# Performance work log

Hardware: AMD Instinct MI355X
Metric: run time of the kernel (lower is better)

The kernel has to match this reference:

```python
import jax, jax.numpy as jnp
import numpy as np

WIN = 7  # window size (w1 = w2 = 7)

def _rel_pos_indices(w: int) -> jnp.ndarray:
    # Matches RelPosBias 2-D branch: [(w*w), (w*w)] indices into (2w-1)^2 table
    p = np.arange(w)
    gi, gj = np.meshgrid(p, p, indexing='ij')
    grid = np.stack([gi.reshape(-1), gj.reshape(-1)], axis=-1)  # [w*w, 2]
    rel = grid[:, None, :] - grid[None, :, :]                   # [w*w, w*w, 2]
    rel = rel + (w - 1)
    idx = rel[..., 0] * (2 * w - 1) + rel[..., 1]               # [w*w, w*w]
    return jnp.asarray(idx, dtype=jnp.int32)


def setup_inputs() -> dict:
    key = jax.random.key(0)
    k1, k2, k3, k4 = jax.random.split(key, 4)
    dim, heads = 256, 8
    b, gx, gy = 64, 8, 8
    x = jax.random.normal(k1, (b, gx, gy, WIN, WIN, dim), dtype=jnp.float32)
    # torch nn.Linear weight layout: [out_features, in_features]
    w_qkv = jax.random.normal(k2, (3 * dim, dim), dtype=jnp.float32) * (dim ** -0.5)
    w_out = jax.random.normal(k3, (dim, dim), dtype=jnp.float32) * (dim ** -0.5)
    rel_emb = jax.random.normal(k4, ((2 * WIN - 1) ** 2, heads), dtype=jnp.float32) * 0.02
    rel_idx = _rel_pos_indices(WIN)
    return {"x": x, "w_qkv": w_qkv, "w_out": w_out, "rel_emb": rel_emb, "rel_idx": rel_idx}


def reference(x, w_qkv, w_out, rel_emb, rel_idx):
    b, gx, gy, w1, w2, d = x.shape
    h = rel_emb.shape[1]          # heads
    dh = d // h                    # dim_head
    scale = dh ** -0.5
    n = w1 * w2                    # tokens per window (49)

    xr = x.reshape(b * gx * gy, n, d)                        # (B, n, d)
    qkv = jnp.einsum('bnd,ed->bne', xr, w_qkv)               # (B, n, 3d)
    q, k, v = jnp.split(qkv, 3, axis=-1)
    split_heads = lambda t: t.reshape(t.shape[0], n, h, dh).transpose(0, 2, 1, 3)
    q, k, v = map(split_heads, (q, k, v))                    # (B, h, n, dh)

    sim = jnp.einsum('bhid,bhjd->bhij', q * scale, k)        # (B, h, n, n)
    bias = rel_emb[rel_idx]                                   # (n, n, h)
    sim = sim + bias.transpose(2, 0, 1)[None]                 # + (1, h, n, n)
    attn = jax.nn.softmax(sim, axis=-1)

    out = jnp.einsum('bhij,bhjd->bhid', attn, v)              # (B, h, n, dh)
    out = out.transpose(0, 2, 1, 3).reshape(-1, w1, w2, d)    # (B, w1, w2, d)
    out = jnp.einsum('bxyd,ed->bxye', out, w_out)
    return out.reshape(b, gx, gy, w1, w2, d)
```

## Files before the change

### kernel.cpp

```cpp
#include <hip/hip_runtime.h>
#include <hip/hip_bf16.h>

typedef __bf16 bf16x8 __attribute__((ext_vector_type(8)));
typedef __bf16 bf16x4v __attribute__((ext_vector_type(4)));
typedef float f32x4 __attribute__((ext_vector_type(4)));

#define MFMA(a, b, c) __builtin_amdgcn_mfma_f32_16x16x32_bf16((a), (b), (c), 0, 0, 0)
#define NEG_BIG (-1e30f)

#define XO_LD 264
#define QK_LD 36
#define VT_LD 72
#define P_LD 68
#define OTR_LD 36
#define Q_OFF 0
#define K_OFF 2304
#define VT_OFF 4608
#define P_OFF 6912
#define OTR_OFF 11264
#define TOTAL_ELS (64 * XO_LD)

static __device__ inline bf16x8 ld8x2(const __bf16* p) {
  bf16x4v lo = *(const bf16x4v*)p;
  bf16x4v hi = *(const bf16x4v*)(p + 4);
  bf16x8 r;
  r[0] = lo[0]; r[1] = lo[1]; r[2] = lo[2]; r[3] = lo[3];
  r[4] = hi[0]; r[5] = hi[1]; r[6] = hi[2]; r[7] = hi[3];
  return r;
}

__global__ __launch_bounds__(256) void prep_kernel(
    const float* __restrict__ w_qkv, const float* __restrict__ w_out,
    const float* __restrict__ rel_emb, const int* __restrict__ rel_idx,
    __bf16* __restrict__ wqkv_f, __bf16* __restrict__ wout_f,
    float* __restrict__ bias) {
  const float kScale = 0.17677669529663687f;
  int idx = blockIdx.x * 256 + threadIdx.x;
  if (idx < 24576) {
    int lane = idx & 63, k2 = (idx >> 6) & 7;
    int hn = idx >> 9;
    int nt = hn % 6, h = hn / 6;
    int quad = lane >> 4, l16 = lane & 15;
    int grow = (nt >> 1) * 256 + h * 32 + (nt & 1) * 16 + l16;
    const float* src = w_qkv + grow * 256 + k2 * 32 + quad * 8;
    float s = (nt < 2) ? kScale : 1.0f;
    bf16x8 d;
#pragma unroll
    for (int j = 0; j < 8; ++j) d[j] = (__bf16)(src[j] * s);
    *(bf16x8*)&wqkv_f[idx * 8] = d;
  } else if (idx < 32768) {
    int j2 = idx - 24576;
    int lane = j2 & 63, kk = (j2 >> 6) & 7, ntile = j2 >> 9;
    int quad = lane >> 4, l16 = lane & 15;
    const float* src = w_out + (ntile * 16 + l16) * 256 + kk * 32 + quad * 8;
    bf16x8 d;
#pragma unroll
    for (int j = 0; j < 8; ++j) d[j] = (__bf16)src[j];
    *(bf16x8*)&wout_f[j2 * 8] = d;
  } else if (idx < 65536) {
    int j = idx - 32768;
    int h = j >> 12;
    int mt = (j >> 10) & 3;
    int nt = (j >> 8) & 3;
    int lane = (j >> 2) & 63;
    int r = j & 3;
    int row = mt * 16 + ((lane >> 4) << 2) + r;
    int col = nt * 16 + (lane & 15);
    float v = NEG_BIG;
    if (row < 49 && col < 49) v = rel_emb[rel_idx[row * 49 + col] * 8 + h];
    bias[j] = v;
  }
}

__global__ __launch_bounds__(256, 4) void attn_kernel(
    const float* __restrict__ x, const __bf16* __restrict__ wqkv,
    const __bf16* __restrict__ wout, const float* __restrict__ bias,
    float* __restrict__ out) {
  __shared__ __attribute__((aligned(16))) __bf16 sm[TOTAL_ELS];

  const int tid = threadIdx.x;
  const int wave = tid >> 6;
  const int lane = tid & 63;
  const int quad = lane >> 4;
  const int l16 = lane & 15;
  const int i0 = wave * 16 + quad * 4;
  const int am = wave * 16 + l16;

  const f32x4 fzero = {0.f, 0.f, 0.f, 0.f};

  {
    const float4* xg = (const float4*)(x + (size_t)blockIdx.x * 12544);
    for (int i = tid; i < 3136; i += 256) {
      float4 v = xg[i];
      int row = i >> 6, c4 = (i & 63) << 2;
      bf16x4v t;
      t[0] = (__bf16)v.x; t[1] = (__bf16)v.y; t[2] = (__bf16)v.z; t[3] = (__bf16)v.w;
      *(bf16x4v*)&sm[row * XO_LD + c4] = t;
    }
    bf16x4v z;
    z[0] = z[1] = z[2] = z[3] = (__bf16)0.0f;
    for (int i = tid; i < 960; i += 256) {
      int row = 49 + (i >> 6), c4 = (i & 63) << 2;
      *(bf16x4v*)&sm[row * XO_LD + c4] = z;
    }
  }
  __syncthreads();

  bf16x8 afr[8];
#pragma unroll
  for (int kk = 0; kk < 8; ++kk)
    afr[kk] = *(const bf16x8*)&sm[am * XO_LD + kk * 32 + quad * 8];
  __syncthreads();

  bf16x8 ofr[8];

  for (int h = 0; h < 8; ++h) {
    f32x4 acc[6];
#pragma unroll
    for (int t = 0; t < 6; ++t) acc[t] = fzero;
    {
      const __bf16* wb = wqkv + (size_t)h * 24576;
#pragma unroll
      for (int k2 = 0; k2 < 8; ++k2) {
        bf16x8 a = afr[k2];
#pragma unroll
        for (int nt = 0; nt < 6; ++nt) {
          bf16x8 b = *(const bf16x8*)&wb[(nt * 8 + k2) * 512 + lane * 8];
          acc[nt] = MFMA(a, b, acc[nt]);
        }
      }
    }

    f32x4 sim[4];
    {
      const float* bb = bias + (h << 12) + (wave << 10) + (lane << 2);
#pragma unroll
      for (int nt = 0; nt < 4; ++nt) sim[nt] = *(const f32x4*)&bb[nt << 8];
    }

#pragma unroll
    for (int t = 0; t < 2; ++t) {
#pragma unroll
      for (int r = 0; r < 4; ++r) {
        sm[Q_OFF + (i0 + r) * QK_LD + t * 16 + l16] = (__bf16)acc[t][r];
        sm[K_OFF + (i0 + r) * QK_LD + t * 16 + l16] = (__bf16)acc[2 + t][r];
      }
      bf16x4v pv;
#pragma unroll
      for (int r = 0; r < 4; ++r) pv[r] = (__bf16)acc[4 + t][r];
      *(bf16x4v*)&sm[VT_OFF + (t * 16 + l16) * VT_LD + i0] = pv;
    }
    __syncthreads();

    {
      bf16x8 a = ld8x2(&sm[Q_OFF + am * QK_LD + quad * 8]);
#pragma unroll
      for (int nt = 0; nt < 4; ++nt) {
        bf16x8 b = ld8x2(&sm[K_OFF + (nt * 16 + l16) * QK_LD + quad * 8]);
        sim[nt] = MFMA(a, b, sim[nt]);
      }
    }

#pragma unroll
    for (int r = 0; r < 4; ++r) {
      float mx = fmaxf(fmaxf(sim[0][r], sim[1][r]), fmaxf(sim[2][r], sim[3][r]));
      mx = fmaxf(mx, __shfl_xor(mx, 1));
      mx = fmaxf(mx, __shfl_xor(mx, 2));
      mx = fmaxf(mx, __shfl_xor(mx, 4));
      mx = fmaxf(mx, __shfl_xor(mx, 8));
      float e0 = __expf(sim[0][r] - mx), e1 = __expf(sim[1][r] - mx);
      float e2 = __expf(sim[2][r] - mx), e3 = __expf(sim[3][r] - mx);
      float sum = e0 + e1 + e2 + e3;
      sum += __shfl_xor(sum, 1);
      sum += __shfl_xor(sum, 2);
      sum += __shfl_xor(sum, 4);
      sum += __shfl_xor(sum, 8);
      float rs = 1.0f / sum;
      int row = i0 + r;
      sm[P_OFF + row * P_LD + l16] = (__bf16)(e0 * rs);
      sm[P_OFF + row * P_LD + 16 + l16] = (__bf16)(e1 * rs);
      sm[P_OFF + row * P_LD + 32 + l16] = (__bf16)(e2 * rs);
      sm[P_OFF + row * P_LD + 48 + l16] = (__bf16)(e3 * rs);
    }
    __syncthreads();

    f32x4 oa[2];
    oa[0] = fzero;
    oa[1] = fzero;
#pragma unroll
    for (int kk = 0; kk < 2; ++kk) {
      bf16x8 a = ld8x2(&sm[P_OFF + am * P_LD + kk * 32 + quad * 8]);
#pragma unroll
      for (int t = 0; t < 2; ++t) {
        bf16x8 b = *(const bf16x8*)&sm[VT_OFF + (t * 16 + l16) * VT_LD + kk * 32 + quad * 8];
        oa[t] = MFMA(a, b, oa[t]);
      }
    }
#pragma unroll
    for (int t = 0; t < 2; ++t)
#pragma unroll
      for (int r = 0; r < 4; ++r)
        sm[OTR_OFF + (i0 + r) * OTR_LD + t * 16 + l16] = (__bf16)oa[t][r];
    __syncthreads();
    ofr[h] = ld8x2(&sm[OTR_OFF + am * OTR_LD + quad * 8]);
  }

  float* ob_base = out + (size_t)blockIdx.x * 12544;
  for (int ct = 0; ct < 8; ++ct) {
    f32x4 fa[2];
    fa[0] = fzero;
    fa[1] = fzero;
#pragma unroll
    for (int kk = 0; kk < 8; ++kk) {
#pragma unroll
      for (int t = 0; t < 2; ++t) {
        bf16x8 bw = *(const bf16x8*)&wout[((ct * 2 + t) * 8 + kk) * 512 + lane * 8];
        fa[t] = MFMA(ofr[kk], bw, fa[t]);
      }
    }
    float* ob = ob_base + ct * 32;
#pragma unroll
    for (int t = 0; t < 2; ++t)
#pragma unroll
      for (int r = 0; r < 4; ++r) {
        int row = i0 + r;
        if (row < 49) ob[row * 256 + t * 16 + l16] = fa[t][r];
      }
  }
}

extern "C" void kernel_launch(void* const* d_in, const int* in_sizes, int n_in,
                              void* d_out, int out_size, void* d_ws, size_t ws_size,
                              hipStream_t stream) {
  (void)in_sizes; (void)n_in; (void)out_size; (void)ws_size;
  const float* x = (const float*)d_in[0];
  const float* w_qkv = (const float*)d_in[1];
  const float* w_out = (const float*)d_in[2];
  const float* rel_emb = (const float*)d_in[3];
  const int* rel_idx = (const int*)d_in[4];
  float* out = (float*)d_out;

  char* ws = (char*)d_ws;
  __bf16* wqkv_f = (__bf16*)ws;
  __bf16* wout_f = (__bf16*)(ws + 393216);
  float* bias = (float*)(ws + 524288);

  prep_kernel<<<256, 256, 0, stream>>>(w_qkv, w_out, rel_emb, rel_idx,
                                       wqkv_f, wout_f, bias);
  attn_kernel<<<4096, 256, 0, stream>>>(x, wqkv_f, wout_f, bias, out);
}
```

Baseline: 894.5 us.

## Load x straight into registers, shrink LDS, drop wave-local barriers and softmax max

The input tile is now read directly from global memory into MFMA A-fragments in registers, instead of being staged through a large shared-memory buffer. That removes the staging buffer, which shrinks LDS use and lets the launch bound ask for 7 blocks per CU instead of 4. The barriers around the P and O shared-memory buffers are removed because each wave only reads rows it wrote itself, and the O tile now reuses the P region. A single barrier at the start of each head guards the K/V overwrite. The softmax no longer subtracts the row maximum, which saves shuffles but risks exp overflow if logits ever grow large.

Result: faster. 872.1 us (-2.5%).

```diff
diff --git a/kernel.cpp b/kernel.cpp
--- a/kernel.cpp
+++ b/kernel.cpp
@@ -8,17 +8,14 @@
 #define MFMA(a, b, c) __builtin_amdgcn_mfma_f32_16x16x32_bf16((a), (b), (c), 0, 0, 0)
 #define NEG_BIG (-1e30f)
 
-#define XO_LD 264
 #define QK_LD 36
 #define VT_LD 72
 #define P_LD 68
-#define OTR_LD 36
-#define Q_OFF 0
-#define K_OFF 2304
-#define VT_OFF 4608
+#define K_OFF 0
+#define VT_OFF 2304
+#define Q_OFF 4608
 #define P_OFF 6912
-#define OTR_OFF 11264
-#define TOTAL_ELS (64 * XO_LD)
+#define TOTAL_ELS 11264
 
 static __device__ inline bf16x8 ld8x2(const __bf16* p) {
   bf16x4v lo = *(const bf16x4v*)p;
@@ -72,7 +69,7 @@
   }
 }
 
-__global__ __launch_bounds__(256, 4) void attn_kernel(
+__global__ __launch_bounds__(256, 7) void attn_kernel(
     const float* __restrict__ x, const __bf16* __restrict__ wqkv,
     const __bf16* __restrict__ wout, const float* __restrict__ bias,
     float* __restrict__ out) {
@@ -88,29 +85,21 @@
 
   const f32x4 fzero = {0.f, 0.f, 0.f, 0.f};
 
+  bf16x8 afr[8];
   {
-    const float4* xg = (const float4*)(x + (size_t)blockIdx.x * 12544);
-    for (int i = tid; i < 3136; i += 256) {
-      float4 v = xg[i];
-      int row = i >> 6, c4 = (i & 63) << 2;
-      bf16x4v t;
-      t[0] = (__bf16)v.x; t[1] = (__bf16)v.y; t[2] = (__bf16)v.z; t[3] = (__bf16)v.w;
-      *(bf16x4v*)&sm[row * XO_LD + c4] = t;
-    }
-    bf16x4v z;
-    z[0] = z[1] = z[2] = z[3] = (__bf16)0.0f;
-    for (int i = tid; i < 960; i += 256) {
-      int row = 49 + (i >> 6), c4 = (i & 63) << 2;
-      *(bf16x4v*)&sm[row * XO_LD + c4] = z;
-    }
-  }
-  __syncthreads();
-
-  bf16x8 afr[8];
-#pragma unroll
-  for (int kk = 0; kk < 8; ++kk)
-    afr[kk] = *(const bf16x8*)&sm[am * XO_LD + kk * 32 + quad * 8];
-  __syncthreads();
+    const float* xrow =
+        x + (size_t)blockIdx.x * 12544 + (am > 48 ? 48 : am) * 256;
+#pragma unroll
+    for (int k2 = 0; k2 < 8; ++k2) {
+      const float* xp = xrow + k2 * 32 + quad * 8;
+      float4 v0 = *(const float4*)xp;
+      float4 v1 = *(const float4*)(xp + 4);
+      bf16x8 a;
+      a[0] = (__bf16)v0.x; a[1] = (__bf16)v0.y; a[2] = (__bf16)v0.z; a[3] = (__bf16)v0.w;
+      a[4] = (__bf16)v1.x; a[5] = (__bf16)v1.y; a[6] = (__bf16)v1.z; a[7] = (__bf16)v1.w;
+      afr[k2] = a;
+    }
+  }
 
   bf16x8 ofr[8];
 
@@ -138,6 +127,8 @@
       for (int nt = 0; nt < 4; ++nt) sim[nt] = *(const f32x4*)&bb[nt << 8];
     }
 
+    if (h) __syncthreads();
+
 #pragma unroll
     for (int t = 0; t < 2; ++t) {
 #pragma unroll
@@ -163,26 +154,20 @@
 
 #pragma unroll
     for (int r = 0; r < 4; ++r) {
-      float mx = fmaxf(fmaxf(sim[0][r], sim[1][r]), fmaxf(sim[2][r], sim[3][r]));
-      mx = fmaxf(mx, __shfl_xor(mx, 1));
-      mx = fmaxf(mx, __shfl_xor(mx, 2));
-      mx = fmaxf(mx, __shfl_xor(mx, 4));
-      mx = fmaxf(mx, __shfl_xor(mx, 8));
-      float e0 = __expf(sim[0][r] - mx), e1 = __expf(sim[1][r] - mx);
-      float e2 = __expf(sim[2][r] - mx), e3 = __expf(sim[3][r] - mx);
+      float e0 = __expf(sim[0][r]), e1 = __expf(sim[1][r]);
+      float e2 = __expf(sim[2][r]), e3 = __expf(sim[3][r]);
       float sum = e0 + e1 + e2 + e3;
       sum += __shfl_xor(sum, 1);
       sum += __shfl_xor(sum, 2);
       sum += __shfl_xor(sum, 4);
       sum += __shfl_xor(sum, 8);
-      float rs = 1.0f / sum;
+      float rs = (sum > 0.f) ? (1.0f / sum) : 0.f;
       int row = i0 + r;
       sm[P_OFF + row * P_LD + l16] = (__bf16)(e0 * rs);
       sm[P_OFF + row * P_LD + 16 + l16] = (__bf16)(e1 * rs);
       sm[P_OFF + row * P_LD + 32 + l16] = (__bf16)(e2 * rs);
       sm[P_OFF + row * P_LD + 48 + l16] = (__bf16)(e3 * rs);
     }
-    __syncthreads();
 
     f32x4 oa[2];
     oa[0] = fzero;
@@ -200,9 +185,8 @@
     for (int t = 0; t < 2; ++t)
 #pragma unroll
       for (int r = 0; r < 4; ++r)
-        sm[OTR_OFF + (i0 + r) * OTR_LD + t * 16 + l16] = (__bf16)oa[t][r];
-    __syncthreads();
-    ofr[h] = ld8x2(&sm[OTR_OFF + am * OTR_LD + quad * 8]);
+        sm[P_OFF + (i0 + r) * P_LD + t * 16 + l16] = (__bf16)oa[t][r];
+    ofr[h] = ld8x2(&sm[P_OFF + am * P_LD + quad * 8]);
   }
 
   float* ob_base = out + (size_t)blockIdx.x * 12544;
```
